# Performance work log

Measured on AMD Instinct MI355X. Metric: run time of the kernel, lower is better.

Reference implementation:

```python
import math
import jax, jax.numpy as jnp
import numpy as np

B, N, D, H, L, TD, KN, KE = 4, 256, 512, 8, 6, 128, 16, 4
DH = D // H
EPS = 1e-5


def _ln(x, g, b):
    m = jnp.mean(x, axis=-1, keepdims=True)
    v = jnp.var(x, axis=-1, keepdims=True)
    return (x - m) * jax.lax.rsqrt(v + EPS) * g + b


def setup_inputs() -> dict:
    key = jax.random.key(0)
    ks = iter(jax.random.split(key, 64))
    s = 0.02
    inp = {
        'x_nodes_t': jax.random.randint(next(ks), (B, N), 0, KN),
        'x_edges_t': jax.random.randint(next(ks), (B, N, N), 0, KE),
        't': jax.random.randint(next(ks), (B,), 0, 1000),
        'c_emb_vec': jax.random.normal(next(ks), (B, D), jnp.float32),
        # embeddings / time MLP
        'node_embed': s * jax.random.normal(next(ks), (KN, D), jnp.float32),
        'time_w1': s * jax.random.normal(next(ks), (TD, D), jnp.float32),
        'time_b1': jnp.zeros((D,), jnp.float32),
        'time_w2': s * jax.random.normal(next(ks), (D, D), jnp.float32),
        'time_b2': jnp.zeros((D,), jnp.float32),
        'edge_bias_tab': s * jax.random.normal(next(ks), (KE, H), jnp.float32),
        # stacked per-layer params [L, ...]
        'ln1_g': jnp.ones((L, D), jnp.float32),
        'ln1_b': jnp.zeros((L, D), jnp.float32),
        'Wq': s * jax.random.normal(next(ks), (L, D, D), jnp.float32),
        'Wk': s * jax.random.normal(next(ks), (L, D, D), jnp.float32),
        'Wv': s * jax.random.normal(next(ks), (L, D, D), jnp.float32),
        'Wo': s * jax.random.normal(next(ks), (L, D, D), jnp.float32),
        'ln2_g': jnp.ones((L, D), jnp.float32),
        'ln2_b': jnp.zeros((L, D), jnp.float32),
        'ff_w1': s * jax.random.normal(next(ks), (L, D, 4 * D), jnp.float32),
        'ff_b1': jnp.zeros((L, 4 * D), jnp.float32),
        'ff_w2': s * jax.random.normal(next(ks), (L, 4 * D, D), jnp.float32),
        'ff_b2': jnp.zeros((L, D), jnp.float32),
        # output heads
        'node_w': s * jax.random.normal(next(ks), (D, KN), jnp.float32),
        'node_b': jnp.zeros((KN,), jnp.float32),
        'pair_w1': s * jax.random.normal(next(ks), (2 * D, D), jnp.float32),
        'pair_b1': jnp.zeros((D,), jnp.float32),
        'pair_w2': s * jax.random.normal(next(ks), (D, KE), jnp.float32),
        'pair_b2': jnp.zeros((KE,), jnp.float32),
    }
    return inp


def _forward(x_nodes_t, x_edges_t, t, c_emb_vec, node_embed, time_w1, time_b1,
             time_w2, time_b2, edge_bias_tab, ln1_g, ln1_b, Wq, Wk, Wv, Wo,
             ln2_g, ln2_b, ff_w1, ff_b1, ff_w2, ff_b2, node_w, node_b,
             pair_w1, pair_b1, pair_w2, pair_b2):
    # sinusoidal time embedding: [B] -> [B, TD]
    half = TD // 2
    freqs = jnp.exp(-math.log(10000.0) * jnp.arange(half, dtype=jnp.float32) / half)
    ang = t.astype(jnp.float32)[:, None] * freqs[None, :]
    temb = jnp.concatenate([jnp.sin(ang), jnp.cos(ang)], axis=-1)
    temb = jax.nn.silu(temb @ time_w1 + time_b1) @ time_w2 + time_b2  # [B, D]

    h = node_embed[x_nodes_t]                      # [B, N, D]
    h = h + temb[:, None, :] + c_emb_vec[:, None, :]

    attn_bias = jnp.transpose(edge_bias_tab[x_edges_t], (0, 3, 1, 2))  # [B, H, N, N]
    scale = DH ** -0.5

    for i in range(L):
        hn = _ln(h, ln1_g[i], ln1_b[i])
        q = (hn @ Wq[i]).reshape(B, N, H, DH)
        k = (hn @ Wk[i]).reshape(B, N, H, DH)
        v = (hn @ Wv[i]).reshape(B, N, H, DH)
        logits = jnp.einsum('bnhd,bmhd->bhnm', q, k) * scale + attn_bias
        a = jax.nn.softmax(logits, axis=-1)
        o = jnp.einsum('bhnm,bmhd->bnhd', a, v).reshape(B, N, D)
        h = h + o @ Wo[i]
        hn2 = _ln(h, ln2_g[i], ln2_b[i])
        h = h + jax.nn.silu(hn2 @ ff_w1[i] + ff_b1[i]) @ ff_w2[i] + ff_b2[i]

    node_logits = h @ node_w + node_b              # [B, N, KN]

    # edge pair MLP: concat([h_i, h_j]) @ W1 == h_i @ W1a + h_j @ W1b (fused form)
    w1a, w1b = pair_w1[:D], pair_w1[D:]
    pa = h @ w1a                                   # [B, N, D]
    pb = h @ w1b                                   # [B, N, D]
    pair = jax.nn.silu(pa[:, :, None, :] + pb[:, None, :, :] + pair_b1)  # [B,N,N,D]
    edge_logits = pair @ pair_w2 + pair_b2         # [B, N, N, KE]

    idx = jnp.arange(N)
    edge_logits = edge_logits.at[:, idx, idx, :].set(-1e9)
    edge_logits = edge_logits.at[:, idx, idx, 0].set(1e9)
    edge_logits = 0.5 * (edge_logits + jnp.transpose(edge_logits, (0, 2, 1, 3)))
    return node_logits, edge_logits


def reference(x_nodes_t, x_edges_t, t, c_emb_vec, node_embed, time_w1, time_b1,
              time_w2, time_b2, edge_bias_tab, ln1_g, ln1_b, Wq, Wk, Wv, Wo,
              ln2_g, ln2_b, ff_w1, ff_b1, ff_w2, ff_b2, node_w, node_b,
              pair_w1, pair_b1, pair_w2, pair_b2):
    return _forward(x_nodes_t, x_edges_t, t, c_emb_vec, node_embed, time_w1,
                    time_b1, time_w2, time_b2, edge_bias_tab, ln1_g, ln1_b,
                    Wq, Wk, Wv, Wo, ln2_g, ln2_b, ff_w1, ff_b1, ff_w2, ff_b2,
                    node_w, node_b, pair_w1, pair_b1, pair_w2, pair_b2)
```

## Files before the change

### kernel.cpp

```cpp
#include <hip/hip_runtime.h>
#include <math.h>

#define BB 4
#define NN 256
#define DD 512
#define HH 8
#define LL 6
#define TDIM 128
#define KNN 16
#define KEE 4
#define DHH 64
#define PSTRIDE ((size_t)BB * NN * NN * KEE)

typedef unsigned short u16;
typedef __bf16 bf16x8 __attribute__((ext_vector_type(8)));
typedef float f32x16 __attribute__((ext_vector_type(16)));
typedef u16 u16x8 __attribute__((ext_vector_type(8)));
typedef u16 u16x4 __attribute__((ext_vector_type(4)));
typedef unsigned int u32;

#define GLOBAL_AS(p) ((__attribute__((address_space(1))) void*)(p))
#define LDS_AS(p)    ((__attribute__((address_space(3))) void*)(p))

__device__ __forceinline__ u16 f2bf(float x) {
    unsigned u = __float_as_uint(x);
    u = (u + 0x7FFFu + ((u >> 16) & 1u)) >> 16;
    return (u16)u;
}
__device__ __forceinline__ float bf2f(u16 x) {
    return __uint_as_float(((unsigned)x) << 16);
}
__device__ __forceinline__ u32 cvtpk_bf16(float lo, float hi) {
    u32 r;
    asm("v_cvt_pk_bf16_f32 %0, %1, %2" : "=v"(r) : "v"(lo), "v"(hi));
    return r;
}

__global__ void temb_kernel(const int* __restrict__ t_in, const float* __restrict__ w1,
                            const float* __restrict__ b1, const float* __restrict__ w2,
                            const float* __restrict__ b2, float* __restrict__ temb)
{
    int b = blockIdx.x;
    int t = threadIdx.x;
    __shared__ float t0[TDIM];
    __shared__ float t1[DD];
    float tv = (float)t_in[b];
    if (t < TDIM) {
        int j = t & 63;
        float fr = expf(-logf(10000.f) * (float)j / 64.f);
        float ang = tv * fr;
        t0[t] = (t < 64) ? sinf(ang) : cosf(ang);
    }
    __syncthreads();
    float acc = b1[t];
    for (int k = 0; k < TDIM; ++k) acc += t0[k] * w1[k * DD + t];
    t1[t] = acc / (1.f + expf(-acc));
    __syncthreads();
    float acc2 = b2[t];
    for (int k = 0; k < DD; ++k) acc2 += t1[k] * w2[k * DD + t];
    temb[b * DD + t] = acc2;
}

__global__ void inith_kernel(const int* __restrict__ xn, const float* __restrict__ ne,
                             const float* __restrict__ temb, const float* __restrict__ cemb,
                             float* __restrict__ h, u16* __restrict__ hbf)
{
    int idx = blockIdx.x * 256 + threadIdx.x;
    int d = idx & (DD - 1);
    int bn = idx >> 9;
    int b = bn >> 8;
    float v = ne[xn[bn] * DD + d] + temb[b * DD + d] + cemb[b * DD + d];
    h[idx] = v;
    hbf[idx] = f2bf(v);
}

struct CvtSeg { const float* src; u16* dst; const float* g; const float* b;
                float* u; float* v; int K, N, tx, ty, nl, base; };
struct CvtTab { CvtSeg s[8]; };

__global__ __launch_bounds__(256) void convert_all(CvtTab tab)
{
    const int tile = blockIdx.x;
    int si = 0;
    #pragma unroll
    for (int s2 = 1; s2 < 8; ++s2) if (tile >= tab.s[s2].base) si = s2;
    const CvtSeg sg = tab.s[si];
    int local = tile - sg.base;
    int per = sg.tx * sg.ty;
    int lay = local / per;
    int rem = local - lay * per;
    int bx = rem % sg.tx, by = rem / sg.tx;
    const int kb = by * 64, nb = bx * 64;
    const size_t zoff = (size_t)lay * sg.K * sg.N;
    const int K = sg.K, N = sg.N;

    __shared__ float s[64][65];
    __shared__ float redu[4][64];
    __shared__ float redv[4][64];
    int t = threadIdx.x;
    int r0 = t >> 4, c0 = (t & 15) * 4;
    #pragma unroll
    for (int i = 0; i < 4; ++i) {
        int row = i * 16 + r0;
        float4 v = *reinterpret_cast<const float4*>(sg.src + zoff + (size_t)(kb + row) * N + nb + c0);
        s[row][c0] = v.x; s[row][c0 + 1] = v.y; s[row][c0 + 2] = v.z; s[row][c0 + 3] = v.w;
    }
    __syncthreads();

    if (sg.g) {
        const float* gp = sg.g + lay * DD + kb;
        const float* bp = sg.b + lay * DD + kb;
        #pragma unroll
        for (int i = 0; i < 4; ++i) {
            int n = i * 16 + r0;
            ushort4 o;
            o.x = f2bf(s[c0 + 0][n] * gp[c0 + 0]); o.y = f2bf(s[c0 + 1][n] * gp[c0 + 1]);
            o.z = f2bf(s[c0 + 2][n] * gp[c0 + 2]); o.w = f2bf(s[c0 + 3][n] * gp[c0 + 3]);
            *reinterpret_cast<ushort4*>(sg.dst + zoff + (size_t)(nb + n) * K + kb + c0) = o;
        }
        int col = t & 63, seg = t >> 6;
        float us = 0.f, vs = 0.f;
        #pragma unroll
        for (int r = 0; r < 16; ++r) {
            int row = seg * 16 + r;
            float w_ = s[row][col];
            us += gp[row] * w_;
            vs += bp[row] * w_;
        }
        redu[seg][col] = us;
        redv[seg][col] = vs;
        __syncthreads();
        if (seg == 0) {
            float ut = redu[0][col] + redu[1][col] + redu[2][col] + redu[3][col];
            float vt = redv[0][col] + redv[1][col] + redv[2][col] + redv[3][col];
            atomicAdd(sg.u + (size_t)lay * N + nb + col, ut);
            atomicAdd(sg.v + (size_t)lay * N + nb + col, vt);
        }
    } else {
        #pragma unroll
        for (int i = 0; i < 4; ++i) {
            int n = i * 16 + r0;
            ushort4 o;
            o.x = f2bf(s[c0 + 0][n]); o.y = f2bf(s[c0 + 1][n]);
            o.z = f2bf(s[c0 + 2][n]); o.w = f2bf(s[c0 + 3][n]);
            *reinterpret_cast<ushort4*>(sg.dst + zoff + (size_t)(nb + n) * K + kb + c0) = o;
        }
    }
}

template<int WM, int WN, int NR, int KS, int MODE, bool BIAS, bool SILU, bool RES, bool OBF, bool HBF>
__global__ __launch_bounds__(WM * WN * 64 * KS) void gemm_mfma(
    const u16* __restrict__ A,
    const u16* __restrict__ B0, const u16* __restrict__ B1, const u16* __restrict__ B2,
    const float* __restrict__ u0, const float* __restrict__ u1, const float* __restrict__ u2,
    const float* __restrict__ v0, const float* __restrict__ v1, const float* __restrict__ v2,
    const float* __restrict__ bias, const float* res,
    void* O0, void* O1, void* O2, u16* hbf,
    int M, int N, int K)
{
    constexpr int BM = WM * 32, BN = WN * NR * 32;
    constexpr int GW = WM * WN;
    constexpr int TH = GW * 64;
    constexpr int ABYTES = BM * 128;
    constexpr int BBYTES = BN * 128;
    constexpr int A16 = ABYTES / 16;
    constexpr int B16 = BBYTES / 16;
    __shared__ char smem[KS * 2 * (ABYTES + BBYTES)];
    __shared__ float statS[MODE == 1 ? BM : 1][2];

    const u16* Bm = B0; void* O = O0;
    const float* Uv = u0; const float* Vv = v0;
    if (blockIdx.z == 1) { Bm = B1; O = O1; Uv = u1; Vv = v1; }
    else if (blockIdx.z == 2) { Bm = B2; O = O2; Uv = u2; Vv = v2; }

    const int t = threadIdx.x;
    const int l = t & 63;
    const int w = t >> 6;
    const int ks = w / GW;
    const int wsub = w - ks * GW;
    const int tl = wsub * 64 + l;
    const int lo = l & 31, hi = l >> 5;
    const int wm = wsub / WN, wn = wsub % WN;
    const int row0 = blockIdx.y * BM;
    const int col0 = blockIdx.x * BN;
    const int NK = K >> 6;
    const int NKh = NK / KS;

    if constexpr (MODE == 1) {
        const int rr = t >> 3, sub = t & 7;
        const u16* hr = A + (size_t)(row0 + rr) * K + sub * 64;
        float s = 0.f, sq = 0.f;
        #pragma unroll
        for (int c = 0; c < 8; ++c) {
            u16x8 hv = *reinterpret_cast<const u16x8*>(hr + c * 8);
            #pragma unroll
            for (int e = 0; e < 8; ++e) { float x = bf2f(hv[e]); s += x; sq += x * x; }
        }
        #pragma unroll
        for (int o = 1; o < 8; o <<= 1) { s += __shfl_xor(s, o); sq += __shfl_xor(sq, o); }
        if (sub == 0) {
            float m = s / (float)K;
            float var = sq / (float)K - m * m;
            statS[rr][0] = m;
            statS[rr][1] = rsqrtf(var + 1e-5f);
        }
    }

    char* gbase = smem + ks * 2 * (ABYTES + BBYTES);

    int aoff[4];
    int boff[NR][4];
    #pragma unroll
    for (int kc = 0; kc < 4; ++kc) {
        int slot = (kc * 2 + hi) ^ (lo & 7);
        aoff[kc] = (wm * 32 + lo) * 128 + slot * 16;
        #pragma unroll
        for (int nr = 0; nr < NR; ++nr)
            boff[nr][kc] = (wn * NR * 32 + nr * 32 + lo) * 128 + slot * 16;
    }

    auto stage = [&](int buf, int kt) {
        const int k0 = kt * 64;
        char* base = gbase + buf * (ABYTES + BBYTES);
        #pragma unroll
        for (int idx = tl; idx < A16; idx += TH) {
            int r = idx >> 3, s = idx & 7;
            int ss = s ^ (r & 7);
            const u16* g = A + (size_t)(row0 + r) * K + k0 + ss * 8;
            __builtin_amdgcn_global_load_lds(GLOBAL_AS(g), LDS_AS(base + (idx - l) * 16), 16, 0, 0);
        }
        #pragma unroll
        for (int idx = tl; idx < B16; idx += TH) {
            int r = idx >> 3, s = idx & 7;
            int ss = s ^ (r & 7);
            const u16* g = Bm + (size_t)(col0 + r) * K + k0 + ss * 8;
            __builtin_amdgcn_global_load_lds(GLOBAL_AS(g), LDS_AS(base + ABYTES + (idx - l) * 16), 16, 0, 0);
        }
    };

    f32x16 acc[NR];
    #pragma unroll
    for (int nr = 0; nr < NR; ++nr)
        #pragma unroll
        for (int i = 0; i < 16; ++i) acc[nr][i] = 0.f;

    stage(0, ks * NKh);
    __syncthreads();
    int cur = 0;
    for (int kk = 0; kk < NKh; ++kk) {
        if (kk + 1 < NKh) stage(cur ^ 1, ks * NKh + kk + 1);
        const char* base = gbase + cur * (ABYTES + BBYTES);
        #pragma unroll
        for (int kc = 0; kc < 4; ++kc) {
            bf16x8 av = *reinterpret_cast<const bf16x8*>(base + aoff[kc]);
            #pragma unroll
            for (int nr = 0; nr < NR; ++nr) {
                bf16x8 bb = *reinterpret_cast<const bf16x8*>(base + ABYTES + boff[nr][kc]);
                acc[nr] = __builtin_amdgcn_mfma_f32_32x32x16_bf16(av, bb, acc[nr], 0, 0, 0);
            }
        }
        __syncthreads();
        cur ^= 1;
    }

    if (KS > 1) {
        float* exch = (float*)smem;
        if (ks > 0) {
            #pragma unroll
            for (int nr = 0; nr < NR; ++nr)
                #pragma unroll
                for (int r = 0; r < 16; ++r)
                    exch[(((ks - 1) * NR + nr) * 16 + r) * TH + tl] = acc[nr][r];
        }
        __syncthreads();
        if (ks != 0) return;
        #pragma unroll
        for (int g2 = 1; g2 < KS; ++g2)
            #pragma unroll
            for (int nr = 0; nr < NR; ++nr)
                #pragma unroll
                for (int r = 0; r < 16; ++r)
                    acc[nr][r] += exch[(((g2 - 1) * NR + nr) * 16 + r) * TH + tl];
    }

    #pragma unroll
    for (int nr = 0; nr < NR; ++nr) {
        int col = col0 + wn * NR * 32 + nr * 32 + lo;
        float bs = BIAS ? bias[col] : 0.f;
        float uu = 0.f, vvv = 0.f;
        if constexpr (MODE == 1) { uu = Uv[col]; vvv = Vv[col]; }
        #pragma unroll
        for (int r = 0; r < 16; ++r) {
            int lr = wm * 32 + (r & 3) + 8 * (r >> 2) + 4 * hi;
            int row = row0 + lr;
            float val = acc[nr][r];
            if constexpr (MODE == 1)
                val = statS[lr][1] * (val - statS[lr][0] * uu) + vvv;
            val += bs;
            if (SILU) val = val / (1.f + __expf(-val));
            size_t o = (size_t)row * N + col;
            if (RES) val += res[o];
            if (OBF) ((u16*)O)[o] = f2bf(val);
            else { ((float*)O)[o] = val; if (HBF) hbf[o] = f2bf(val); }
        }
    }
}

__global__ __launch_bounds__(256) void attn_kernel(
    const u16* __restrict__ q8, const u16* __restrict__ k8, const u16* __restrict__ v8,
    const int* __restrict__ xe, const float* __restrict__ tab, u16* __restrict__ o)
{
    const int qt = blockIdx.x * 32, hh = blockIdx.y, b = blockIdx.z;
    const int t = threadIdx.x;
    const int l = t & 63, w = t >> 6;
    const int lo = l & 31, hi = l >> 5;

    __shared__ u16 Ks[NN * 64];
    __shared__ u16 Qs[32 * 64];
    __shared__ u16 Vt[64 * NN];
    __shared__ float opart[4][32 * 64];
    __shared__ float sums[4][32];
    __shared__ float tabs[KEE * HH];

    #pragma unroll
    for (int c = 0; c < 8; ++c) {
        int idx = c * 256 + t;
        int r = idx >> 3, s = idx & 7;
        int ss = s ^ (r & 7);
        const u16* g = k8 + ((size_t)(b * NN + r) * HH + hh) * DHH + ss * 8;
        __builtin_amdgcn_global_load_lds(GLOBAL_AS(g), LDS_AS((char*)Ks + (idx - l) * 16), 16, 0, 0);
    }
    {
        int r = t >> 3, s = t & 7;
        int ss = s ^ (r & 7);
        const u16* g = q8 + ((size_t)(b * NN + qt + r) * HH + hh) * DHH + ss * 8;
        __builtin_amdgcn_global_load_lds(GLOBAL_AS(g), LDS_AS((char*)Qs + (t - l) * 16), 16, 0, 0);
    }
    if (t < KEE * HH) tabs[t] = tab[t];

    {
        const int d0 = (t & 7) * 8, k0 = (t >> 3) * 8;
        u16x8 va[8];
        #pragma unroll
        for (int i = 0; i < 8; ++i)
            va[i] = *reinterpret_cast<const u16x8*>(v8 + ((size_t)(b * NN + k0 + i) * HH + hh) * DHH + d0);
        #pragma unroll
        for (int j = 0; j < 8; ++j) {
            u16x8 tj;
            #pragma unroll
            for (int i = 0; i < 8; ++i) tj[i] = va[i][j];
            int d = d0 + j;
            int slot = (k0 >> 3) ^ (d & 31);
            *reinterpret_cast<u16x8*>(&Vt[d * 256 + slot * 8]) = tj;
        }
    }
    __syncthreads();

    f32x16 acc[2];
    #pragma unroll
    for (int i = 0; i < 2; ++i)
        #pragma unroll
        for (int r = 0; r < 16; ++r) acc[i][r] = 0.f;

    #pragma unroll
    for (int kc = 0; kc < 4; ++kc) {
        int qslot = (kc * 2 + hi) ^ (lo & 7);
        bf16x8 bq = *reinterpret_cast<const bf16x8*>((char*)Qs + lo * 128 + qslot * 16);
        #pragma unroll
        for (int ktl = 0; ktl < 2; ++ktl) {
            int key = (2 * w + ktl) * 32 + lo;
            int kslot = (kc * 2 + hi) ^ (key & 7);
            bf16x8 ak = *reinterpret_cast<const bf16x8*>((char*)Ks + key * 128 + kslot * 16);
            acc[ktl] = __builtin_amdgcn_mfma_f32_32x32x16_bf16(ak, bq, acc[ktl], 0, 0, 0);
        }
    }

    const int qrow = qt + lo;
    const int* xerow = xe + (size_t)(b * NN + qrow) * NN;
    float psum = 0.f;
    #pragma unroll
    for (int ktl = 0; ktl < 2; ++ktl) {
        #pragma unroll
        for (int r = 0; r < 16; ++r) {
            int key = w * 64 + ktl * 32 + (r & 3) + 8 * (r >> 2) + 4 * hi;
            int e = xerow[key];
            float p = __expf(acc[ktl][r] * 0.125f + tabs[e * HH + hh]);
            acc[ktl][r] = p;
            psum += p;
        }
    }
    psum += __shfl_xor(psum, 32);
    if (hi == 0) sums[w][lo] = psum;

    f32x16 oacc[2];
    #pragma unroll
    for (int i = 0; i < 2; ++i)
        #pragma unroll
        for (int r = 0; r < 16; ++r) oacc[i][r] = 0.f;

    #pragma unroll
    for (int kc = 0; kc < 4; ++kc) {
        const int ai = kc >> 1;
        const int s0 = 8 * (kc & 1);
        u32 W0p = cvtpk_bf16(acc[ai][s0 + 0], acc[ai][s0 + 1]);
        u32 W1p = cvtpk_bf16(acc[ai][s0 + 2], acc[ai][s0 + 3]);
        u32 X0p = cvtpk_bf16(acc[ai][s0 + 4], acc[ai][s0 + 5]);
        u32 X1p = cvtpk_bf16(acc[ai][s0 + 6], acc[ai][s0 + 7]);
        u32 z0 = hi ? W0p : X0p;
        u32 z1 = hi ? W1p : X1p;
        u32 r0 = __shfl_xor((int)z0, 32);
        u32 r1 = __shfl_xor((int)z1, 32);
        u32 F[4];
        F[0] = hi ? r0 : W0p;
        F[1] = hi ? r1 : W1p;
        F[2] = hi ? X0p : r0;
        F[3] = hi ? X1p : r1;
        bf16x8 pf = *reinterpret_cast<const bf16x8*>(F);
        #pragma unroll
        for (int nt = 0; nt < 2; ++nt) {
            int d = nt * 32 + lo;
            int slot = (8 * w + kc * 2 + hi) ^ (d & 31);
            bf16x8 vf = *reinterpret_cast<const bf16x8*>(&Vt[d * 256 + slot * 8]);
            oacc[nt] = __builtin_amdgcn_mfma_f32_32x32x16_bf16(pf, vf, oacc[nt], 0, 0, 0);
        }
    }

    #pragma unroll
    for (int nt = 0; nt < 2; ++nt)
        #pragma unroll
        for (int r = 0; r < 16; ++r) {
            int q = (r & 3) + 8 * (r >> 2) + 4 * hi;
            opart[w][q * 64 + nt * 32 + lo] = oacc[nt][r];
        }
    __syncthreads();

    {
        const int q = t >> 3, dd0 = (t & 7) * 8;
        float denom = sums[0][q] + sums[1][q] + sums[2][q] + sums[3][q];
        float rc = __builtin_amdgcn_rcpf(denom);
        u16x8 o8;
        #pragma unroll
        for (int j = 0; j < 8; ++j) {
            float s = opart[0][q * 64 + dd0 + j] + opart[1][q * 64 + dd0 + j]
                    + opart[2][q * 64 + dd0 + j] + opart[3][q * 64 + dd0 + j];
            o8[j] = f2bf(s * rc);
        }
        *reinterpret_cast<u16x8*>(o + ((size_t)(b * NN + qt + q) * HH + hh) * DHH + dd0) = o8;
    }
}

__global__ __launch_bounds__(256) void nodelogits_kernel(const float* __restrict__ h,
                                                         const float* __restrict__ nw,
                                                         const float* __restrict__ nb,
                                                         float* __restrict__ out)
{
    int row = blockIdx.x;
    int t = threadIdx.x;
    int kk = t & 15, seg = t >> 4;
    const float* hr = h + (size_t)row * DD;
    float acc = 0.f;
    #pragma unroll 8
    for (int d = seg * 32; d < seg * 32 + 32; ++d) acc += hr[d] * nw[d * KNN + kk];
    __shared__ float sm[16][17];
    sm[seg][kk] = acc;
    __syncthreads();
    if (t < KNN) {
        float s = 0.f;
        #pragma unroll
        for (int g2 = 0; g2 < 16; ++g2) s += sm[g2][t];
        out[(size_t)row * KNN + t] = s + nb[t];
    }
}

__global__ __launch_bounds__(256) void pair_kernel(
    const u16* __restrict__ pa8, const u16* __restrict__ pb8,
    const float* __restrict__ b1, const float* __restrict__ w2,
    float* __restrict__ etmp)
{
    const int jt = blockIdx.x * 32, it = blockIdx.y * 32;
    const int b = blockIdx.z >> 1, half = blockIdx.z & 1;
    const int t = threadIdx.x;
    const int j2 = t & 15, i2 = t >> 4;

    __shared__ float pas[32][132];
    __shared__ float pbs[32][132];
    __shared__ float4 w2s[128];

    float4 acc00 = {0,0,0,0}, acc01 = {0,0,0,0}, acc10 = {0,0,0,0}, acc11 = {0,0,0,0};

    for (int c2 = 0; c2 < 2; ++c2) {
        const int d0 = (half * 2 + c2) * 128;
        if (c2) __syncthreads();
        #pragma unroll
        for (int c = 0; c < 2; ++c) {
            int qd = c * 256 + t;
            int r = qd >> 4, part = (qd & 15) * 8;
            u16x8 av = *reinterpret_cast<const u16x8*>(pa8 + (size_t)(b * NN + it + r) * DD + d0 + part);
            u16x8 bv = *reinterpret_cast<const u16x8*>(pb8 + (size_t)(b * NN + jt + r) * DD + d0 + part);
            float4 b1a = *reinterpret_cast<const float4*>(b1 + d0 + part);
            float4 b1b = *reinterpret_cast<const float4*>(b1 + d0 + part + 4);
            *reinterpret_cast<float4*>(&pas[r][part]) =
                make_float4(bf2f(av[0]) + b1a.x, bf2f(av[1]) + b1a.y, bf2f(av[2]) + b1a.z, bf2f(av[3]) + b1a.w);
            *reinterpret_cast<float4*>(&pas[r][part + 4]) =
                make_float4(bf2f(av[4]) + b1b.x, bf2f(av[5]) + b1b.y, bf2f(av[6]) + b1b.z, bf2f(av[7]) + b1b.w);
            *reinterpret_cast<float4*>(&pbs[r][part]) =
                make_float4(bf2f(bv[0]), bf2f(bv[1]), bf2f(bv[2]), bf2f(bv[3]));
            *reinterpret_cast<float4*>(&pbs[r][part + 4]) =
                make_float4(bf2f(bv[4]), bf2f(bv[5]), bf2f(bv[6]), bf2f(bv[7]));
        }
        if (t < 128) w2s[t] = *reinterpret_cast<const float4*>(w2 + (size_t)(d0 + t) * KEE);
        __syncthreads();

        #pragma unroll 4
        for (int dq = 0; dq < 32; ++dq) {
            float4 paA = *reinterpret_cast<const float4*>(&pas[i2][dq * 4]);
            float4 paB = *reinterpret_cast<const float4*>(&pas[i2 + 16][dq * 4]);
            float4 pbA = *reinterpret_cast<const float4*>(&pbs[j2][dq * 4]);
            float4 pbB = *reinterpret_cast<const float4*>(&pbs[j2 + 16][dq * 4]);
            float4 w0 = w2s[dq * 4], w1 = w2s[dq * 4 + 1], w2v = w2s[dq * 4 + 2], w3 = w2s[dq * 4 + 3];

            #define HSILU(x) ((x) * __builtin_amdgcn_fmed3f(__builtin_fmaf((x), 0.25f, 0.5f), 0.f, 1.f))
            #define PAIR_STEP(ACC, PA, PB)                                                     \
            {                                                                                  \
                float s0 = HSILU(PA.x + PB.x), s1 = HSILU(PA.y + PB.y);                        \
                float s2 = HSILU(PA.z + PB.z), s3 = HSILU(PA.w + PB.w);                        \
                ACC.x += s0 * w0.x + s1 * w1.x + s2 * w2v.x + s3 * w3.x;                       \
                ACC.y += s0 * w0.y + s1 * w1.y + s2 * w2v.y + s3 * w3.y;                       \
                ACC.z += s0 * w0.z + s1 * w1.z + s2 * w2v.z + s3 * w3.z;                       \
                ACC.w += s0 * w0.w + s1 * w1.w + s2 * w2v.w + s3 * w3.w;                       \
            }
            PAIR_STEP(acc00, paA, pbA)
            PAIR_STEP(acc01, paA, pbB)
            PAIR_STEP(acc10, paB, pbA)
            PAIR_STEP(acc11, paB, pbB)
            #undef PAIR_STEP
            #undef HSILU
        }
    }

    float* ep = etmp + half * PSTRIDE;
    #define WRITE(ACC, I, J)                                                                   \
        *reinterpret_cast<float4*>(ep + (((size_t)(b * NN + (I)) * NN) + (J)) * KEE) =         \
            make_float4(ACC.x, ACC.y, ACC.z, ACC.w);
    WRITE(acc00, it + i2,      jt + j2)
    WRITE(acc01, it + i2,      jt + j2 + 16)
    WRITE(acc10, it + i2 + 16, jt + j2)
    WRITE(acc11, it + i2 + 16, jt + j2 + 16)
    #undef WRITE
}

__global__ void symm_kernel(const float* __restrict__ et, const float* __restrict__ b2,
                            float* __restrict__ out)
{
    int idx = blockIdx.x * 256 + threadIdx.x;
    int j = idx & 255;
    int i = (idx >> 8) & 255;
    int b = idx >> 16;
    size_t fwd = (size_t)idx * KEE;
    size_t rev = (((size_t)b * NN + j) * NN + i) * KEE;
    float4 r4;
    if (i == j) {
        r4 = make_float4(1e9f, -1e9f, -1e9f, -1e9f);
    } else {
        float4 a0 = *reinterpret_cast<const float4*>(et + fwd);
        float4 a1 = *reinterpret_cast<const float4*>(et + PSTRIDE + fwd);
        float4 c0 = *reinterpret_cast<const float4*>(et + rev);
        float4 c1 = *reinterpret_cast<const float4*>(et + PSTRIDE + rev);
        r4 = make_float4(0.5f * (a0.x + a1.x + c0.x + c1.x) + b2[0],
                         0.5f * (a0.y + a1.y + c0.y + c1.y) + b2[1],
                         0.5f * (a0.z + a1.z + c0.z + c1.z) + b2[2],
                         0.5f * (a0.w + a1.w + c0.w + c1.w) + b2[3]);
    }
    *reinterpret_cast<float4*>(out + (size_t)BB * NN * KNN + fwd) = r4;
}

extern "C" void kernel_launch(void* const* d_in, const int* in_sizes, int n_in,
                              void* d_out, int out_size, void* d_ws, size_t ws_size,
                              hipStream_t stream)
{
    const int*   xn   = (const int*)d_in[0];
    const int*   xe   = (const int*)d_in[1];
    const int*   tt   = (const int*)d_in[2];
    const float* cemb = (const float*)d_in[3];
    const float* ne   = (const float*)d_in[4];
    const float* tw1  = (const float*)d_in[5];
    const float* tb1  = (const float*)d_in[6];
    const float* tw2  = (const float*)d_in[7];
    const float* tb2  = (const float*)d_in[8];
    const float* tab  = (const float*)d_in[9];
    const float* ln1g = (const float*)d_in[10];
    const float* ln1b = (const float*)d_in[11];
    const float* Wq   = (const float*)d_in[12];
    const float* Wk   = (const float*)d_in[13];
    const float* Wv   = (const float*)d_in[14];
    const float* Wo   = (const float*)d_in[15];
    const float* ln2g = (const float*)d_in[16];
    const float* ln2b = (const float*)d_in[17];
    const float* fw1  = (const float*)d_in[18];
    const float* fb1  = (const float*)d_in[19];
    const float* fw2  = (const float*)d_in[20];
    const float* fb2  = (const float*)d_in[21];
    const float* nw   = (const float*)d_in[22];
    const float* nb   = (const float*)d_in[23];
    const float* pw1  = (const float*)d_in[24];
    const float* pb1  = (const float*)d_in[25];
    const float* pw2  = (const float*)d_in[26];
    const float* pb2  = (const float*)d_in[27];
    float* out = (float*)d_out;

    char* wsb = (char*)d_ws;
    size_t off = 0;
    auto alloc = [&](size_t bytes) { char* p = wsb + off; off += (bytes + 255) & ~(size_t)255; return p; };

    float* temb = (float*)alloc(BB * DD * 4);
    float* h    = (float*)alloc((size_t)BB * NN * DD * 4);
    u16* hbf    = (u16*)alloc((size_t)BB * NN * DD * 2);
    u16* pa8    = (u16*)alloc((size_t)BB * NN * DD * 2);
    u16* pb8    = (u16*)alloc((size_t)BB * NN * DD * 2);
    u16* q8     = (u16*)alloc((size_t)BB * NN * DD * 2);
    u16* k8     = (u16*)alloc((size_t)BB * NN * DD * 2);
    u16* v8     = (u16*)alloc((size_t)BB * NN * DD * 2);
    u16* obf    = (u16*)alloc((size_t)BB * NN * DD * 2);
    u16* ff_bf  = (u16*)alloc((size_t)BB * NN * 4 * DD * 2);
    float* et   = (float*)alloc(2 * PSTRIDE * 4);
    u16* wqT    = (u16*)alloc((size_t)LL * DD * DD * 2);
    u16* wkT    = (u16*)alloc((size_t)LL * DD * DD * 2);
    u16* wvT    = (u16*)alloc((size_t)LL * DD * DD * 2);
    u16* woT    = (u16*)alloc((size_t)LL * DD * DD * 2);
    u16* fw1T   = (u16*)alloc((size_t)LL * DD * 4 * DD * 2);
    u16* fw2T   = (u16*)alloc((size_t)LL * DD * 4 * DD * 2);
    u16* pw1aT  = (u16*)alloc((size_t)DD * DD * 2);
    u16* pw1bT  = (u16*)alloc((size_t)DD * DD * 2);
    float* uq   = (float*)alloc((size_t)LL * DD * 4);
    float* vq   = (float*)alloc((size_t)LL * DD * 4);
    float* uk   = (float*)alloc((size_t)LL * DD * 4);
    float* vk   = (float*)alloc((size_t)LL * DD * 4);
    float* uvv  = (float*)alloc((size_t)LL * DD * 4);
    float* vvv  = (float*)alloc((size_t)LL * DD * 4);
    float* uf1  = (float*)alloc((size_t)LL * 4 * DD * 4);
    float* vf1  = (float*)alloc((size_t)LL * 4 * DD * 4);

    const int M = BB * NN;

    size_t foldBytes = (size_t)(6 * LL * DD + 2 * LL * 4 * DD) * 4 + 8 * 256;
    hipMemsetAsync(uq, 0, foldBytes, stream);

    CvtTab tb;
    tb.s[0] = { Wq,  wqT,  ln1g, ln1b, uq,  vq,  DD,     DD,     8,  8,  LL, 0    };
    tb.s[1] = { Wk,  wkT,  ln1g, ln1b, uk,  vk,  DD,     DD,     8,  8,  LL, 384  };
    tb.s[2] = { Wv,  wvT,  ln1g, ln1b, uvv, vvv, DD,     DD,     8,  8,  LL, 768  };
    tb.s[3] = { Wo,  woT,  nullptr, nullptr, nullptr, nullptr, DD, DD, 8, 8, LL, 1152 };
    tb.s[4] = { fw1, fw1T, ln2g, ln2b, uf1, vf1, DD,     4 * DD, 32, 8,  LL, 1536 };
    tb.s[5] = { fw2, fw2T, nullptr, nullptr, nullptr, nullptr, 4 * DD, DD, 8, 32, LL, 3072 };
    tb.s[6] = { pw1,                   pw1aT, nullptr, nullptr, nullptr, nullptr, DD, DD, 8, 8, 1, 4608 };
    tb.s[7] = { pw1 + (size_t)DD * DD, pw1bT, nullptr, nullptr, nullptr, nullptr, DD, DD, 8, 8, 1, 4672 };
    convert_all<<<4736, 256, 0, stream>>>(tb);

    temb_kernel<<<BB, DD, 0, stream>>>(tt, tw1, tb1, tw2, tb2, temb);
    inith_kernel<<<(BB * NN * DD) / 256, 256, 0, stream>>>(xn, ne, temb, cemb, h, hbf);

    for (int l = 0; l < LL; ++l) {
        size_t wo512 = (size_t)l * DD * DD;
        size_t wo2k  = (size_t)l * DD * 4 * DD;
        gemm_mfma<2, 2, 2, 2, 1, false, false, false, true, false><<<dim3(DD / 128, M / 64, 3), 512, 0, stream>>>(
            hbf, wqT + wo512, wkT + wo512, wvT + wo512,
            uq + l * DD, uk + l * DD, uvv + l * DD,
            vq + l * DD, vk + l * DD, vvv + l * DD,
            nullptr, nullptr, q8, k8, v8, nullptr, M, DD, DD);
        attn_kernel<<<dim3(8, HH, BB), 256, 0, stream>>>(q8, k8, v8, xe, tab, obf);
        gemm_mfma<1, 2, 1, 2, 0, false, false, true, false, true><<<dim3(DD / 64, M / 32, 1), 256, 0, stream>>>(
            obf, woT + wo512, nullptr, nullptr,
            nullptr, nullptr, nullptr, nullptr, nullptr, nullptr,
            nullptr, h, h, nullptr, nullptr, hbf, M, DD, DD);
        gemm_mfma<2, 2, 2, 2, 1, true, true, false, true, false><<<dim3(4 * DD / 128, M / 64, 1), 512, 0, stream>>>(
            hbf, fw1T + wo2k, nullptr, nullptr,
            uf1 + (size_t)l * 4 * DD, nullptr, nullptr,
            vf1 + (size_t)l * 4 * DD, nullptr, nullptr,
            fb1 + (size_t)l * 4 * DD, nullptr, ff_bf, nullptr, nullptr, nullptr, M, 4 * DD, DD);
        gemm_mfma<1, 2, 1, 2, 0, true, false, true, false, true><<<dim3(DD / 64, M / 32, 1), 256, 0, stream>>>(
            ff_bf, fw2T + wo2k, nullptr, nullptr,
            nullptr, nullptr, nullptr, nullptr, nullptr, nullptr,
            fb2 + (size_t)l * DD, h, h, nullptr, nullptr, hbf, M, DD, 4 * DD);
    }

    nodelogits_kernel<<<M, 256, 0, stream>>>(h, nw, nb, out);

    gemm_mfma<1, 2, 1, 2, 0, false, false, false, true, false><<<dim3(DD / 64, M / 32, 2), 256, 0, stream>>>(
        hbf, pw1aT, pw1bT, nullptr,
        nullptr, nullptr, nullptr, nullptr, nullptr, nullptr,
        nullptr, nullptr, pa8, pb8, nullptr, nullptr, M, DD, DD);

    pair_kernel<<<dim3(8, 8, BB * 2), 256, 0, stream>>>(pa8, pb8, pb1, pw2, et);
    symm_kernel<<<(BB * NN * NN) / 256, 256, 0, stream>>>(et, pb2, out);

    (void)in_sizes; (void)n_in; (void)out_size; (void)ws_size;
}
```

Measured before the change: 441.3 us.

## Compute layernorm row statistics in residual GEMM epilogues instead of recomputing

The residual-producing GEMMs (Wo and FF2) and the initial h builder now write per-row partial sums and sums of squares into a small stats buffer. The LN-folded GEMMs read these 16 partials per row instead of rereading the full bf16 row of A to compute mean and variance. This removes a redundant row reduction pass in the prologue of every LN-consuming GEMM. The cost is extra shuffles and stores in the epilogues. Statistics now come from fp32 values rather than the bf16 copy, which shifts numerics slightly.

```diff
diff --git a/kernel.cpp b/kernel.cpp
--- a/kernel.cpp
+++ b/kernel.cpp
@@ -61,17 +61,34 @@
     temb[b * DD + t] = acc2;
 }
 
-__global__ void inith_kernel(const int* __restrict__ xn, const float* __restrict__ ne,
-                             const float* __restrict__ temb, const float* __restrict__ cemb,
-                             float* __restrict__ h, u16* __restrict__ hbf)
-{
-    int idx = blockIdx.x * 256 + threadIdx.x;
-    int d = idx & (DD - 1);
-    int bn = idx >> 9;
-    int b = bn >> 8;
-    float v = ne[xn[bn] * DD + d] + temb[b * DD + d] + cemb[b * DD + d];
-    h[idx] = v;
-    hbf[idx] = f2bf(v);
+__global__ __launch_bounds__(256) void inith_kernel(
+    const int* __restrict__ xn, const float* __restrict__ ne,
+    const float* __restrict__ temb, const float* __restrict__ cemb,
+    float* __restrict__ h, u16* __restrict__ hbf, float* __restrict__ statH)
+{
+    int row = blockIdx.x;
+    int b = row >> 8;
+    int t = threadIdx.x;
+    int node = xn[row];
+    float v0 = ne[(size_t)node * DD + t]       + temb[b * DD + t]       + cemb[b * DD + t];
+    float v1 = ne[(size_t)node * DD + t + 256] + temb[b * DD + t + 256] + cemb[b * DD + t + 256];
+    h[(size_t)row * DD + t] = v0;
+    h[(size_t)row * DD + t + 256] = v1;
+    hbf[(size_t)row * DD + t] = f2bf(v0);
+    hbf[(size_t)row * DD + t + 256] = f2bf(v1);
+
+    float s = v0 + v1, q = v0 * v0 + v1 * v1;
+    #pragma unroll
+    for (int o = 32; o; o >>= 1) { s += __shfl_down(s, o); q += __shfl_down(q, o); }
+    __shared__ float ps[4][2];
+    int w = t >> 6, lane = t & 63;
+    if (!lane) { ps[w][0] = s; ps[w][1] = q; }
+    __syncthreads();
+    if (t == 0) {
+        statH[(size_t)row * 32 + 0] = ps[0][0] + ps[1][0] + ps[2][0] + ps[3][0];
+        statH[(size_t)row * 32 + 1] = ps[0][1] + ps[1][1] + ps[2][1] + ps[3][1];
+    }
+    if (t >= 2 && t < 32) statH[(size_t)row * 32 + t] = 0.f;
 }
 
 struct CvtSeg { const float* src; u16* dst; const float* g; const float* b;
@@ -148,14 +165,16 @@
     }
 }
 
-template<int WM, int WN, int NR, int KS, int MODE, bool BIAS, bool SILU, bool RES, bool OBF, bool HBF>
+template<int WM, int WN, int NR, int KS, int MODE, bool BIAS, bool SILU, bool RES, bool OBF,
+         bool HBF, bool STAT>
 __global__ __launch_bounds__(WM * WN * 64 * KS) void gemm_mfma(
     const u16* __restrict__ A,
     const u16* __restrict__ B0, const u16* __restrict__ B1, const u16* __restrict__ B2,
     const float* __restrict__ u0, const float* __restrict__ u1, const float* __restrict__ u2,
     const float* __restrict__ v0, const float* __restrict__ v1, const float* __restrict__ v2,
+    const float* __restrict__ statIn,
     const float* __restrict__ bias, const float* res,
-    void* O0, void* O1, void* O2, u16* hbf,
+    void* O0, void* O1, void* O2, u16* hbf, float* statOut,
     int M, int N, int K)
 {
     constexpr int BM = WM * 32, BN = WN * NR * 32;
@@ -187,22 +206,15 @@
     const int NKh = NK / KS;
 
     if constexpr (MODE == 1) {
-        const int rr = t >> 3, sub = t & 7;
-        const u16* hr = A + (size_t)(row0 + rr) * K + sub * 64;
-        float s = 0.f, sq = 0.f;
-        #pragma unroll
-        for (int c = 0; c < 8; ++c) {
-            u16x8 hv = *reinterpret_cast<const u16x8*>(hr + c * 8);
+        if (t < BM) {
+            const float* sp = statIn + (size_t)(row0 + t) * 32;
+            float s = 0.f, q = 0.f;
             #pragma unroll
-            for (int e = 0; e < 8; ++e) { float x = bf2f(hv[e]); s += x; sq += x * x; }
-        }
-        #pragma unroll
-        for (int o = 1; o < 8; o <<= 1) { s += __shfl_xor(s, o); sq += __shfl_xor(sq, o); }
-        if (sub == 0) {
+            for (int i = 0; i < 16; ++i) { s += sp[i * 2]; q += sp[i * 2 + 1]; }
             float m = s / (float)K;
-            float var = sq / (float)K - m * m;
-            statS[rr][0] = m;
-            statS[rr][1] = rsqrtf(var + 1e-5f);
+            float var = q / (float)K - m * m;
+            statS[t][0] = m;
+            statS[t][1] = rsqrtf(var + 1e-5f);
         }
     }
 
@@ -282,6 +294,8 @@
                 for (int r = 0; r < 16; ++r)
                     acc[nr][r] += exch[(((g2 - 1) * NR + nr) * 16 + r) * TH + tl];
     }
+
+    float v16[STAT ? 16 : 1];
 
     #pragma unroll
     for (int nr = 0; nr < NR; ++nr) {
@@ -302,6 +316,23 @@
             if (RES) val += res[o];
             if (OBF) ((u16*)O)[o] = f2bf(val);
             else { ((float*)O)[o] = val; if (HBF) hbf[o] = f2bf(val); }
+            if constexpr (STAT) v16[r] = val;
+        }
+    }
+
+    if constexpr (STAT) {
+        #pragma unroll
+        for (int r = 0; r < 16; ++r) {
+            float s = v16[r];
+            float q = s * s;
+            #pragma unroll
+            for (int o2 = 1; o2 < 32; o2 <<= 1) { s += __shfl_xor(s, o2); q += __shfl_xor(q, o2); }
+            if (lo == 0) {
+                int row = row0 + wm * 32 + (r & 3) + 8 * (r >> 2) + 4 * hi;
+                int slot = blockIdx.x * 2 + wn;
+                statOut[(size_t)row * 32 + slot * 2 + 0] = s;
+                statOut[(size_t)row * 32 + slot * 2 + 1] = q;
+            }
         }
     }
 }
@@ -615,6 +646,7 @@
     float* temb = (float*)alloc(BB * DD * 4);
     float* h    = (float*)alloc((size_t)BB * NN * DD * 4);
     u16* hbf    = (u16*)alloc((size_t)BB * NN * DD * 2);
+    float* statH = (float*)alloc((size_t)BB * NN * 32 * 4);
     u16* pa8    = (u16*)alloc((size_t)BB * NN * DD * 2);
     u16* pb8    = (u16*)alloc((size_t)BB * NN * DD * 2);
     u16* q8     = (u16*)alloc((size_t)BB * NN * DD * 2);
@@ -657,38 +689,44 @@
     convert_all<<<4736, 256, 0, stream>>>(tb);
 
     temb_kernel<<<BB, DD, 0, stream>>>(tt, tw1, tb1, tw2, tb2, temb);
-    inith_kernel<<<(BB * NN * DD) / 256, 256, 0, stream>>>(xn, ne, temb, cemb, h, hbf);
+    inith_kernel<<<M, 256, 0, stream>>>(xn, ne, temb, cemb, h, hbf, statH);
 
     for (int l = 0; l < LL; ++l) {
         size_t wo512 = (size_t)l * DD * DD;
         size_t wo2k  = (size_t)l * DD * 4 * DD;
-        gemm_mfma<2, 2, 2, 2, 1, false, false, false, true, false><<<dim3(DD / 128, M / 64, 3), 512, 0, stream>>>(
+        gemm_mfma<2, 2, 2, 2, 1, false, false, false, true, false, false>
+            <<<dim3(DD / 128, M / 64, 3), 512, 0, stream>>>(
             hbf, wqT + wo512, wkT + wo512, wvT + wo512,
             uq + l * DD, uk + l * DD, uvv + l * DD,
             vq + l * DD, vk + l * DD, vvv + l * DD,
-            nullptr, nullptr, q8, k8, v8, nullptr, M, DD, DD);
+            statH, nullptr, nullptr, q8, k8, v8, nullptr, nullptr, M, DD, DD);
         attn_kernel<<<dim3(8, HH, BB), 256, 0, stream>>>(q8, k8, v8, xe, tab, obf);
-        gemm_mfma<1, 2, 1, 2, 0, false, false, true, false, true><<<dim3(DD / 64, M / 32, 1), 256, 0, stream>>>(
+        gemm_mfma<1, 2, 1, 2, 0, false, false, true, false, true, true>
+            <<<dim3(DD / 64, M / 32, 1), 256, 0, stream>>>(
             obf, woT + wo512, nullptr, nullptr,
             nullptr, nullptr, nullptr, nullptr, nullptr, nullptr,
-            nullptr, h, h, nullptr, nullptr, hbf, M, DD, DD);
-        gemm_mfma<2, 2, 2, 2, 1, true, true, false, true, false><<<dim3(4 * DD / 128, M / 64, 1), 512, 0, stream>>>(
+            nullptr, nullptr, h, h, nullptr, nullptr, hbf, statH, M, DD, DD);
+        gemm_mfma<2, 2, 2, 2, 1, true, true, false, true, false, false>
+            <<<dim3(4 * DD / 128, M / 64, 1), 512, 0, stream>>>(
             hbf, fw1T + wo2k, nullptr, nullptr,
             uf1 + (size_t)l * 4 * DD, nullptr, nullptr,
             vf1 + (size_t)l * 4 * DD, nullptr, nullptr,
-            fb1 + (size_t)l * 4 * DD, nullptr, ff_bf, nullptr, nullptr, nullptr, M, 4 * DD, DD);
-        gemm_mfma<1, 2, 1, 2, 0, true, false, true, false, true><<<dim3(DD / 64, M / 32, 1), 256, 0, stream>>>(
+            statH, fb1 + (size_t)l * 4 * DD, nullptr, ff_bf, nullptr, nullptr, nullptr, nullptr,
+            M, 4 * DD, DD);
+        gemm_mfma<1, 2, 1, 2, 0, true, false, true, false, true, true>
+            <<<dim3(DD / 64, M / 32, 1), 256, 0, stream>>>(
             ff_bf, fw2T + wo2k, nullptr, nullptr,
             nullptr, nullptr, nullptr, nullptr, nullptr, nullptr,
-            fb2 + (size_t)l * DD, h, h, nullptr, nullptr, hbf, M, DD, 4 * DD);
+            nullptr, fb2 + (size_t)l * DD, h, h, nullptr, nullptr, hbf, statH, M, DD, 4 * DD);
     }
 
     nodelogits_kernel<<<M, 256, 0, stream>>>(h, nw, nb, out);
 
-    gemm_mfma<1, 2, 1, 2, 0, false, false, false, true, false><<<dim3(DD / 64, M / 32, 2), 256, 0, stream>>>(
+    gemm_mfma<1, 2, 1, 2, 0, false, false, false, true, false, false>
+        <<<dim3(DD / 64, M / 32, 2), 256, 0, stream>>>(
         hbf, pw1aT, pw1bT, nullptr,
         nullptr, nullptr, nullptr, nullptr, nullptr, nullptr,
-        nullptr, nullptr, pa8, pb8, nullptr, nullptr, M, DD, DD);
+        nullptr, nullptr, nullptr, pa8, pb8, nullptr, nullptr, nullptr, M, DD, DD);
 
     pair_kernel<<<dim3(8, 8, BB * 2), 256, 0, stream>>>(pa8, pb8, pb1, pw2, et);
     symm_kernel<<<(BB * NN * NN) / 256, 256, 0, stream>>>(et, pb2, out);
```

New measurement: 451.9 us. 2.4% more time.
